# Kernel tuning notes

Measured on AMD Instinct MI355X. Metric: run time of the kernel, lower is better.

## Reference

```python
import jax, jax.numpy as jnp
import numpy as np

B, N, FEAT, H, E, L = 4096, 64, 32, 128, 4, 3  # batch, node_num, node feat, hidden_dim, edge_dim, hidden_num


def setup_inputs() -> dict:
    key = jax.random.key(0)
    ks = jax.random.split(key, 12)
    s = 0.05
    x = jax.random.normal(ks[0], (B, N, FEAT), dtype=jnp.float32)
    adj = jax.random.uniform(ks[1], (B, E, N, N), dtype=jnp.float32)
    # per-node input/output embeddings (stacked over node index)
    in_w = jax.random.normal(ks[2], (N, FEAT, H), dtype=jnp.float32) * s
    in_b = jax.random.normal(ks[3], (N, H), dtype=jnp.float32) * s
    out_w = jax.random.normal(ks[4], (N, H, FEAT), dtype=jnp.float32) * s
    out_b = jax.random.normal(ks[5], (N, FEAT), dtype=jnp.float32) * s
    # relational GC weights per layer: (L, E, H, H) and bias (L, E, 1, H)
    gc_w = jax.random.normal(ks[6], (L, E, H, H), dtype=jnp.float32) * s
    gc_b = jax.random.normal(ks[7], (L, E, 1, H), dtype=jnp.float32) * s
    # GRU params, gate order [r, z, n] like torch
    w_ih = jax.random.normal(ks[8], (3 * H, H), dtype=jnp.float32) * s
    w_hh = jax.random.normal(ks[9], (3 * H, H), dtype=jnp.float32) * s
    b_ih = jax.random.normal(ks[10], (3 * H,), dtype=jnp.float32) * s
    b_hh = jax.random.normal(ks[11], (3 * H,), dtype=jnp.float32) * s
    return {"x": x, "adj": adj, "in_w": in_w, "in_b": in_b, "out_w": out_w,
            "out_b": out_b, "gc_w": gc_w, "gc_b": gc_b, "w_ih": w_ih,
            "w_hh": w_hh, "b_ih": b_ih, "b_hh": b_hh}


def _gru_step(xf, h, w_ih, w_hh, b_ih, b_hh):
    # xf, h: (B*N, H); single-timestep torch GRU cell
    gi = xf @ w_ih.T + b_ih
    gh = h @ w_hh.T + b_hh
    i_r, i_z, i_n = jnp.split(gi, 3, axis=-1)
    h_r, h_z, h_n = jnp.split(gh, 3, axis=-1)
    r = jax.nn.sigmoid(i_r + h_r)
    z = jax.nn.sigmoid(i_z + h_z)
    n = jnp.tanh(i_n + r * h_n)
    return (1.0 - z) * n + z * h


def reference(x, adj, in_w, in_b, out_w, out_b, gc_w, gc_b, w_ih, w_hh, b_ih, b_hh):
    # per-node input embedding: (B, N, FEAT) -> (B, N, H)
    h = jnp.einsum('bnd,ndh->bnh', x, in_w) + in_b
    hidden = h.reshape(-1, H)  # initial GRU hidden = embedded input
    cur = h
    for i in range(L):
        # relational GCN: per-edge-type projection + adjacency matmul + bias + relu + mean over edge types
        support = jnp.einsum('bid,edh->beih', cur, gc_w[i])
        out = jnp.einsum('beij,bejh->beih', adj, support) + gc_b[i]
        out = jax.nn.relu(out)
        agg = jnp.mean(out, axis=1)  # (B, N, H)
        hidden = _gru_step(agg.reshape(-1, H), hidden, w_ih, w_hh, b_ih, b_hh)
        cur = hidden.reshape(B, N, H)
    # per-node output embedding, zero-padded back to hidden width
    feats = jnp.einsum('bnh,nhd->bnd', cur, out_w) + out_b  # (B, N, FEAT)
    return jnp.pad(feats, ((0, 0), (0, 0), (0, H - FEAT)))
```

## Files before the change

### kernel.cpp

```cpp
#include <hip/hip_runtime.h>
#include <cstdint>

#define NBATCH 4096
#define NNODE  64
#define FEAT   32
#define H      128
#define NE     4
#define NL     3

typedef __attribute__((ext_vector_type(8))) short short8;
typedef __attribute__((ext_vector_type(4))) short short4v;
typedef __attribute__((ext_vector_type(4))) float f32x4;
typedef __attribute__((ext_vector_type(2))) float f32x2;
typedef unsigned long long u64;

#define IMG_GC_ELEMS   (128 * 64)
#define IMG_GRU_ELEMS  (48 * 128)
#define IMG_GC_BYTES   (24 * IMG_GC_ELEMS * 2)
#define IMG_GRU_BYTES  (16 * IMG_GRU_ELEMS * 2)
#define WS_W_BYTES     (IMG_GC_BYTES + IMG_GRU_BYTES)
#define WIMG_SHORTS    (WS_W_BYTES / 2)
#define ADJ_IMG_ELEMS  4096
#define WS_FULL ((size_t)WS_W_BYTES + (size_t)NBATCH * NE * ADJ_IMG_ELEMS * 2)

__device__ __forceinline__ unsigned short f2b(float f) {
  union { float f; unsigned u; } v; v.f = f;
  unsigned u = v.u + 0x7FFFu + ((v.u >> 16) & 1u);
  return (unsigned short)(u >> 16);
}
__device__ __forceinline__ float b2f(unsigned short s) {
  union { unsigned u; float f; } v; v.u = ((unsigned)s) << 16;
  return v.f;
}
__device__ __forceinline__ unsigned cvtpk(float lo, float hi) {
  unsigned r;
  asm volatile("v_cvt_pk_bf16_f32 %0, %1, %2" : "=v"(r) : "v"(lo), "v"(hi));
  return r;
}
__device__ __forceinline__ float sigm(float v) { return 1.0f / (1.0f + __expf(-v)); }
__device__ __forceinline__ float tanh_(float v) {
  v = fminf(fmaxf(v, -15.f), 15.f);
  float e = __expf(-2.f * v);
  return (1.f - e) / (1.f + e);
}
__device__ __forceinline__ int gidx128(int r, int g) { return r * 128 + ((g ^ (r & 7)) << 3); }
__device__ __forceinline__ int idx128(int r, int k) { return gidx128(r, k >> 3) + (k & 7); }
__device__ __forceinline__ int gidx64(int r, int g) { return r * 64 + (((g ^ (r & 7)) & 7) << 3); }

__device__ __forceinline__ short8 pack8f(const float* v) {
  union { unsigned u[4]; short8 s; } r;
  r.u[0] = cvtpk(v[0], v[1]); r.u[1] = cvtpk(v[2], v[3]);
  r.u[2] = cvtpk(v[4], v[5]); r.u[3] = cvtpk(v[6], v[7]);
  return r.s;
}

__device__ __forceinline__ void gll16(const void* g, void* l) {
  __builtin_amdgcn_global_load_lds(
      (const __attribute__((address_space(1))) unsigned int*)g,
      (__attribute__((address_space(3))) unsigned int*)l, 16, 0, 0);
}

#define STAGE(dst, src, NIT)                                             \
  do {                                                                   \
    _Pragma("unroll")                                                    \
    for (int it_ = 0; it_ < (NIT); ++it_) {                              \
      int off_ = (it_ * 4 + w) * 1024;                                   \
      gll16((const char*)(src) + off_ + lane * 16, (char*)(dst) + off_); \
    }                                                                    \
  } while (0)

#define BAR() do { asm volatile("s_waitcnt lgkmcnt(0)" ::: "memory"); \
                   __builtin_amdgcn_s_barrier(); } while (0)
#define VMW(N) do { asm volatile("s_waitcnt vmcnt(" #N ")" ::: "memory"); \
                    __builtin_amdgcn_sched_barrier(0); } while (0)
#define SB0() __builtin_amdgcn_sched_barrier(0)

__global__ __launch_bounds__(256, 2) void k_prep(
    const float* __restrict__ gc_w, const float* __restrict__ w_ih,
    const float* __restrict__ w_hh, unsigned short* __restrict__ ws)
{
  const int t = threadIdx.x;
  if (blockIdx.x < 24) {
    const int blk = blockIdx.x;
    const int kh = blk & 1, e = (blk >> 1) & 3, l = blk >> 3;
    const float* We = gc_w + (size_t)(l * NE + e) * H * H;
    unsigned short* dst = ws + (size_t)blk * IMG_GC_ELEMS;
    #pragma unroll
    for (int it = 0; it < 4; ++it) {
      int idx = t + it * 256;
      int r = idx >> 3, g = idx & 7;
      float v[8];
      #pragma unroll
      for (int j = 0; j < 8; ++j) v[j] = We[(kh * 64 + g * 8 + j) * H + r];
      *(short8*)&dst[gidx64(r, g)] = pack8f(v);
    }
  } else {
    const int blk = blockIdx.x - 24;
    const int c = blk & 7, m = blk >> 3;
    const float* Mat = m ? w_hh : w_ih;
    unsigned short* dst = ws + WIMG_SHORTS - IMG_GRU_BYTES / 2 + (size_t)blk * IMG_GRU_ELEMS;
    #pragma unroll
    for (int it = 0; it < 3; ++it) {
      int idx = t + it * 256;
      int rr = idx >> 4, g = idx & 15;
      int mrow = (rr >> 4) * H + 16 * c + (rr & 15);
      float v[8];
      #pragma unroll
      for (int j = 0; j < 8; ++j) v[j] = Mat[mrow * H + g * 8 + j];
      *(short8*)&dst[gidx128(rr, g)] = pack8f(v);
    }
  }
}

template <bool ADJIMG>
__global__ __launch_bounds__(256, 2) void k_inemb(
    const float* __restrict__ x, const float* __restrict__ in_w,
    const float* __restrict__ in_b, const float* __restrict__ adj,
    unsigned short* __restrict__ ws, float* __restrict__ out)
{
  __shared__ float s_wt[FEAT * H];
  __shared__ float s_x[64 * FEAT];
  const int t = threadIdx.x;
  const int n = blockIdx.x >> 6, bt = blockIdx.x & 63, b0 = bt * 64;
  const float* wsrc = in_w + (size_t)n * FEAT * H;
  #pragma unroll
  for (int it = 0; it < 4; ++it) {
    int i4 = t + it * 256;
    *(f32x4*)&s_wt[i4 * 4] = *(const f32x4*)&wsrc[i4 * 4];
  }
  {
    int r = t >> 2, q = t & 3;
    const float* xs = x + ((size_t)(b0 + r) * NNODE + n) * FEAT;
    *(f32x4*)&s_x[r * 32 + q * 8]     = *(const f32x4*)&xs[q * 8];
    *(f32x4*)&s_x[r * 32 + q * 8 + 4] = *(const f32x4*)&xs[q * 8 + 4];
  }
  __syncthreads();
  const int h2 = t & 63, rp = t >> 6;
  const float bi0 = in_b[n * H + 2 * h2], bi1 = in_b[n * H + 2 * h2 + 1];
  #pragma unroll 1
  for (int m = 0; m < 16; ++m) {
    int r = rp + 4 * m;
    float a0 = bi0, a1 = bi1;
    #pragma unroll
    for (int d = 0; d < 32; ++d) {
      float xv = s_x[r * 32 + d];
      f32x2 wv = *(const f32x2*)&s_wt[d * H + 2 * h2];
      a0 += xv * wv.x; a1 += xv * wv.y;
    }
    unsigned p = cvtpk(a0, a1);
    unsigned short* tail = (unsigned short*)(out + ((size_t)(b0 + r) * NNODE + n) * H + 64);
    *(unsigned*)(tail + 2 * h2) = p;
  }
  if (ADJIMG) {
    const float* ab = adj + (size_t)blockIdx.x * NE * NNODE * NNODE;
    unsigned short* dst = ws + WIMG_SHORTS + (size_t)blockIdx.x * NE * ADJ_IMG_ELEMS;
    #pragma unroll 1
    for (int q = 0; q < 8; ++q) {
      int gi = t + q * 256;
      int e = gi >> 9, idx = gi & 511, r = idx >> 3, g = idx & 7;
      const float* src = ab + e * 4096 + r * 64 + g * 8;
      float v[8];
      #pragma unroll
      for (int j = 0; j < 8; ++j) v[j] = src[j];
      *(short8*)&dst[e * ADJ_IMG_ELEMS + gidx64(r, g)] = pack8f(v);
    }
  }
}

template <bool ADJIMG>
__global__ __launch_bounds__(256, 2) void k_main(
    const float* __restrict__ adj,
    const float* __restrict__ gc_b,
    const float* __restrict__ b_ih, const float* __restrict__ b_hh,
    const unsigned short* __restrict__ wimg,
    float* __restrict__ out)
{
  __shared__ unsigned short s_cur[64 * 128];
  __shared__ unsigned short s_u[128 * 64];
  __shared__ unsigned short s_w0[128 * 64];
  __shared__ unsigned short s_w1[128 * 64];
  __shared__ unsigned short s_adj[64 * 64];
  __shared__ float s_bias[1280];

  const int t = threadIdx.x;
  const int b = blockIdx.x;
  const int w = t >> 6, lane = t & 63, lr = lane & 15, lq = lane >> 4;
  float* outb = out + (size_t)b * NNODE * H;
  const unsigned short* img_gru = wimg + WIMG_SHORTS - IMG_GRU_BYTES / 2;
  const unsigned short* aimg = wimg + WIMG_SHORTS + (size_t)b * NE * ADJ_IMG_ELEMS;

  STAGE(s_w0, wimg, 4);
  #pragma unroll
  for (int it = 0; it < 4; ++it) {
    int idx = t + it * 256;
    int n = idx >> 4, g = idx & 15;
    short8 v = *(const short8*)((const unsigned short*)(outb + n * H + 64) + g * 8);
    *(short8*)&s_cur[gidx128(n, g)] = v;
  }
  #pragma unroll
  for (int it = 0; it < 3; ++it) {
    int idx = t + it * 256;
    s_bias[512 + idx] = (idx < 384) ? b_ih[idx] : b_hh[idx - 384];
  }
  __syncthreads();

  #pragma unroll 1
  for (int layer = 0; layer < NL; ++layer) {
    f32x4 agg[8];
    #pragma unroll
    for (int tn = 0; tn < 8; ++tn) agg[tn] = f32x4{0.f, 0.f, 0.f, 0.f};

    #pragma unroll 1
    for (int e = 0; e < NE; ++e) {
      const unsigned short* img_e = wimg + (size_t)((layer * NE + e) * 2) * IMG_GC_ELEMS;

      if (e == 0) {
        s_bias[t]       = gc_b[layer * 512 + t];
        s_bias[t + 256] = gc_b[layer * 512 + t + 256];
      }
      STAGE(s_w1, img_e + IMG_GC_ELEMS, 4);
      SB0();
      if (ADJIMG) {
        STAGE(s_adj, aimg + (size_t)e * ADJ_IMG_ELEMS, 2);
        SB0();
      } else {
        const float* adj_e = adj + (((size_t)b * NE + e) * NNODE * NNODE);
        #pragma unroll
        for (int it = 0; it < 2; ++it) {
          int idx = t + it * 256;
          int i = idx >> 3, g = idx & 7;
          const float* src = adj_e + i * 64 + g * 8;
          float v[8];
          #pragma unroll
          for (int j = 0; j < 8; ++j) v[j] = src[j];
          *(short8*)&s_adj[gidx64(i, g)] = pack8f(v);
        }
      }
      f32x4 Sacc[8];
      #pragma unroll
      for (int tn = 0; tn < 8; ++tn) Sacc[tn] = f32x4{0.f, 0.f, 0.f, 0.f};
      __builtin_amdgcn_s_setprio(1);
      #pragma unroll
      for (int ks = 0; ks < 2; ++ks) {
        short8 a = *(const short8*)&s_cur[gidx128(16 * w + lr, ks * 4 + lq)];
        #pragma unroll
        for (int tn = 0; tn < 8; ++tn) {
          short8 bb = *(const short8*)&s_w0[gidx64(16 * tn + lr, ks * 4 + lq)];
          Sacc[tn] = __builtin_amdgcn_mfma_f32_16x16x32_bf16(a, bb, Sacc[tn], 0, 0, 0);
        }
      }
      __builtin_amdgcn_s_setprio(0);
      if (ADJIMG) { VMW(2); }
      else        { VMW(0); }
      BAR();

      if (e < 3) { STAGE(s_w0, img_e + 2 * IMG_GC_ELEMS, 4); }
      else       { STAGE(s_w0, img_gru, 3); }
      SB0();
      __builtin_amdgcn_s_setprio(1);
      #pragma unroll
      for (int ks = 0; ks < 2; ++ks) {
        short8 a = *(const short8*)&s_cur[gidx128(16 * w + lr, 8 + ks * 4 + lq)];
        #pragma unroll
        for (int tn = 0; tn < 8; ++tn) {
          short8 bb = *(const short8*)&s_w1[gidx64(16 * tn + lr, ks * 4 + lq)];
          Sacc[tn] = __builtin_amdgcn_mfma_f32_16x16x32_bf16(a, bb, Sacc[tn], 0, 0, 0);
        }
      }
      __builtin_amdgcn_s_setprio(0);
      {
        int nb = 16 * w + 4 * lq;
        int g = nb >> 3, sub = nb & 7;
        #pragma unroll
        for (int tn = 0; tn < 8; ++tn) {
          int h = 16 * tn + lr;
          u64 pv = (u64)cvtpk(Sacc[tn][0], Sacc[tn][1]) |
                   ((u64)cvtpk(Sacc[tn][2], Sacc[tn][3]) << 32);
          *(u64*)&s_u[gidx64(h, g) + sub] = pv;
        }
      }
      VMW(4);
      BAR();

      {
        f32x4 Oacc[8];
        #pragma unroll
        for (int tn = 0; tn < 8; ++tn) Oacc[tn] = f32x4{0.f, 0.f, 0.f, 0.f};
        __builtin_amdgcn_s_setprio(1);
        #pragma unroll
        for (int ks = 0; ks < 2; ++ks) {
          short8 a = *(const short8*)&s_adj[gidx64(16 * w + lr, ks * 4 + lq)];
          #pragma unroll
          for (int tn = 0; tn < 8; ++tn) {
            short8 bb = *(const short8*)&s_u[gidx64(16 * tn + lr, ks * 4 + lq)];
            Oacc[tn] = __builtin_amdgcn_mfma_f32_16x16x32_bf16(a, bb, Oacc[tn], 0, 0, 0);
          }
        }
        __builtin_amdgcn_s_setprio(0);
        #pragma unroll
        for (int tn = 0; tn < 8; ++tn) {
          float bias = s_bias[e * 128 + 16 * tn + lr];
          #pragma unroll
          for (int r = 0; r < 4; ++r)
            agg[tn][r] += 0.25f * fmaxf(Oacc[tn][r] + bias, 0.f);
        }
      }
      VMW(0);
      BAR();
    }

    #pragma unroll
    for (int tn = 0; tn < 8; ++tn) {
      int h = 16 * tn + lr;
      #pragma unroll
      for (int r = 0; r < 4; ++r) {
        int i = 16 * w + 4 * lq + r;
        s_u[idx128(i, h)] = f2b(agg[tn][r]);
      }
    }
    BAR();

    #pragma unroll 1
    for (int c = 0; c < 8; ++c) {
      STAGE(s_w1, img_gru + (size_t)(8 + c) * IMG_GRU_ELEMS, 3);
      f32x4 gi[3], gh[3];
      #pragma unroll
      for (int tg = 0; tg < 3; ++tg) gi[tg] = f32x4{0.f, 0.f, 0.f, 0.f};
      __builtin_amdgcn_s_setprio(1);
      #pragma unroll
      for (int ks = 0; ks < 4; ++ks) {
        short8 bb = *(const short8*)&s_u[gidx128(16 * w + lr, ks * 4 + lq)];
        #pragma unroll
        for (int tg = 0; tg < 3; ++tg) {
          short8 a = *(const short8*)&s_w0[gidx128(16 * tg + lr, ks * 4 + lq)];
          gi[tg] = __builtin_amdgcn_mfma_f32_16x16x32_bf16(a, bb, gi[tg], 0, 0, 0);
        }
      }
      __builtin_amdgcn_s_setprio(0);
      __syncthreads();

      if (c < 7)          { STAGE(s_w0, img_gru + (size_t)(c + 1) * IMG_GRU_ELEMS, 3); }
      else if (layer < 2) { STAGE(s_w0, wimg + (size_t)((layer + 1) * NE * 2) * IMG_GC_ELEMS, 4); }
      #pragma unroll
      for (int tg = 0; tg < 3; ++tg) gh[tg] = f32x4{0.f, 0.f, 0.f, 0.f};
      __builtin_amdgcn_s_setprio(1);
      #pragma unroll
      for (int ks = 0; ks < 4; ++ks) {
        short8 bb = *(const short8*)&s_cur[gidx128(16 * w + lr, ks * 4 + lq)];
        #pragma unroll
        for (int tg = 0; tg < 3; ++tg) {
          short8 a = *(const short8*)&s_w1[gidx128(16 * tg + lr, ks * 4 + lq)];
          gh[tg] = __builtin_amdgcn_mfma_f32_16x16x32_bf16(a, bb, gh[tg], 0, 0, 0);
        }
      }
      __builtin_amdgcn_s_setprio(0);
      {
        int i = 16 * w + lr;
        int g = (16 * c + 4 * lq) >> 3;
        int off = gidx128(i, g) + ((4 * lq) & 7);
        short4v hv = *(const short4v*)&s_cur[off];
        float hf[4];
        #pragma unroll
        for (int r = 0; r < 4; ++r) {
          int mH = 16 * c + 4 * lq + r;
          float rg = sigm(gi[0][r] + s_bias[512 + mH] + gh[0][r] + s_bias[896 + mH]);
          float zg = sigm(gi[1][r] + s_bias[640 + mH] + gh[1][r] + s_bias[1024 + mH]);
          float ng = tanh_(gi[2][r] + s_bias[768 + mH] + rg * (gh[2][r] + s_bias[1152 + mH]));
          float hold = b2f((unsigned short)hv[r]);
          hf[r] = (1.f - zg) * ng + zg * hold;
        }
        u64 hp = (u64)cvtpk(hf[0], hf[1]) | ((u64)cvtpk(hf[2], hf[3]) << 32);
        unsigned short* tail = (unsigned short*)(outb + (size_t)i * H + 64);
        *(u64*)(tail + 16 * c + 4 * lq) = hp;
      }
      __syncthreads();
    }

    if (layer < 2) {
      #pragma unroll
      for (int it = 0; it < 4; ++it) {
        int idx = t + it * 256;
        int n = idx >> 4, g = idx & 15;
        short8 v = *(const short8*)((const unsigned short*)(outb + n * H + 64) + g * 8);
        *(short8*)&s_cur[gidx128(n, g)] = v;
      }
      __syncthreads();
    }
  }
}

__global__ __launch_bounds__(256, 2) void k_outemb(
    const float* __restrict__ out_w, const float* __restrict__ out_b,
    float* __restrict__ out)
{
  __shared__ float s_wt[H * FEAT];
  __shared__ float s_c[64 * 132];
  const int t = threadIdx.x;
  const int n = blockIdx.x >> 6, bt = blockIdx.x & 63, b0 = bt * 64;
  const float* wsrc = out_w + (size_t)n * H * FEAT;
  #pragma unroll
  for (int it = 0; it < 4; ++it) {
    int i4 = t + it * 256;
    *(f32x4*)&s_wt[i4 * 4] = *(const f32x4*)&wsrc[i4 * 4];
  }
  #pragma unroll
  for (int it = 0; it < 4; ++it) {
    int idx = t + it * 256;
    int r = idx >> 4, g = idx & 15;
    const unsigned short* tail =
        (const unsigned short*)(out + ((size_t)(b0 + r) * NNODE + n) * H + 64);
    short8 v = *(const short8*)(tail + g * 8);
    #pragma unroll
    for (int j = 0; j < 8; ++j) s_c[r * 132 + g * 8 + j] = b2f((unsigned short)v[j]);
  }
  __syncthreads();
  const int d = t & 31, rq = t >> 5;
  const float bias = out_b[n * FEAT + d];
  float accs[8];
  #pragma unroll
  for (int m = 0; m < 8; ++m) {
    int r = rq + 8 * m;
    float a = bias;
    #pragma unroll 8
    for (int k = 0; k < H; ++k) a += s_c[r * 132 + k] * s_wt[k * FEAT + d];
    accs[m] = a;
  }
  #pragma unroll
  for (int m = 0; m < 8; ++m) {
    int r = rq + 8 * m;
    out[((size_t)(b0 + r) * NNODE + n) * H + d] = accs[m];
  }
  #pragma unroll
  for (int q = 0; q < 6; ++q) {
    int idx = t + q * 256;
    int r = idx / 24, c4 = idx - r * 24;
    *(f32x4*)&out[((size_t)(b0 + r) * NNODE + n) * H + FEAT + c4 * 4] =
        f32x4{0.f, 0.f, 0.f, 0.f};
  }
}

extern "C" void kernel_launch(void* const* d_in, const int* in_sizes, int n_in,
                              void* d_out, int out_size, void* d_ws, size_t ws_size,
                              hipStream_t stream) {
  const float* x     = (const float*)d_in[0];
  const float* adj   = (const float*)d_in[1];
  const float* in_w  = (const float*)d_in[2];
  const float* in_b  = (const float*)d_in[3];
  const float* out_w = (const float*)d_in[4];
  const float* out_b = (const float*)d_in[5];
  const float* gc_w  = (const float*)d_in[6];
  const float* gc_b  = (const float*)d_in[7];
  const float* w_ih  = (const float*)d_in[8];
  const float* w_hh  = (const float*)d_in[9];
  const float* b_ih  = (const float*)d_in[10];
  const float* b_hh  = (const float*)d_in[11];
  (void)in_sizes; (void)n_in; (void)out_size;
  unsigned short* wimg = (unsigned short*)d_ws;
  const bool full = ws_size >= WS_FULL;
  hipLaunchKernelGGL(k_prep, dim3(40), dim3(256), 0, stream, gc_w, w_ih, w_hh, wimg);
  if (full) {
    hipLaunchKernelGGL(k_inemb<true>, dim3(NBATCH), dim3(256), 0, stream,
                       x, in_w, in_b, adj, wimg, (float*)d_out);
    hipLaunchKernelGGL(k_main<true>, dim3(NBATCH), dim3(256), 0, stream,
                       adj, gc_b, b_ih, b_hh, wimg, (float*)d_out);
  } else {
    hipLaunchKernelGGL(k_inemb<false>, dim3(NBATCH), dim3(256), 0, stream,
                       x, in_w, in_b, adj, wimg, (float*)d_out);
    hipLaunchKernelGGL(k_main<false>, dim3(NBATCH), dim3(256), 0, stream,
                       adj, gc_b, b_ih, b_hh, wimg, (float*)d_out);
  }
  hipLaunchKernelGGL(k_outemb, dim3(NBATCH), dim3(256), 0, stream, out_w, out_b, (float*)d_out);
}
```

Before: 823.8 us.

## Retile main kernel MFMAs into 2x2 warp grid with register-held current state

The per-warp work split in the main GCN/GRU kernel changes from 16-row strips over all columns to a 2x2 warp grid (32 rows by 64 columns per warp), so each B fragment loaded from LDS feeds two MFMAs. The current hidden state is kept in registers instead of an LDS tile. The GRU loop now processes two weight chunks per iteration, with separate warp pairs handling each. LDS buffers are merged into one aliased staging area with adjusted vmcnt waits. This aims to cut LDS traffic and barriers, and the smaller LDS footprint may allow more occupancy. In exchange it raises register pressure and makes the async-copy wait counts more fragile.

```diff
diff --git a/kernel.cpp b/kernel.cpp
--- a/kernel.cpp
+++ b/kernel.cpp
@@ -13,6 +13,7 @@
 typedef __attribute__((ext_vector_type(4))) float f32x4;
 typedef __attribute__((ext_vector_type(2))) float f32x2;
 typedef unsigned long long u64;
+typedef unsigned short ushort;
 
 #define IMG_GC_ELEMS   (128 * 64)
 #define IMG_GRU_ELEMS  (48 * 128)
@@ -23,12 +24,12 @@
 #define ADJ_IMG_ELEMS  4096
 #define WS_FULL ((size_t)WS_W_BYTES + (size_t)NBATCH * NE * ADJ_IMG_ELEMS * 2)
 
-__device__ __forceinline__ unsigned short f2b(float f) {
+__device__ __forceinline__ ushort f2b(float f) {
   union { float f; unsigned u; } v; v.f = f;
   unsigned u = v.u + 0x7FFFu + ((v.u >> 16) & 1u);
-  return (unsigned short)(u >> 16);
-}
-__device__ __forceinline__ float b2f(unsigned short s) {
+  return (ushort)(u >> 16);
+}
+__device__ __forceinline__ float b2f(ushort s) {
   union { unsigned u; float f; } v; v.u = ((unsigned)s) << 16;
   return v.f;
 }
@@ -36,6 +37,9 @@
   unsigned r;
   asm volatile("v_cvt_pk_bf16_f32 %0, %1, %2" : "=v"(r) : "v"(lo), "v"(hi));
   return r;
+}
+__device__ __forceinline__ u64 pk4(float a, float b, float c, float d) {
+  return (u64)cvtpk(a, b) | ((u64)cvtpk(c, d) << 32);
 }
 __device__ __forceinline__ float sigm(float v) { return 1.0f / (1.0f + __expf(-v)); }
 __device__ __forceinline__ float tanh_(float v) {
@@ -77,14 +81,14 @@
 
 __global__ __launch_bounds__(256, 2) void k_prep(
     const float* __restrict__ gc_w, const float* __restrict__ w_ih,
-    const float* __restrict__ w_hh, unsigned short* __restrict__ ws)
+    const float* __restrict__ w_hh, ushort* __restrict__ ws)
 {
   const int t = threadIdx.x;
   if (blockIdx.x < 24) {
     const int blk = blockIdx.x;
     const int kh = blk & 1, e = (blk >> 1) & 3, l = blk >> 3;
     const float* We = gc_w + (size_t)(l * NE + e) * H * H;
-    unsigned short* dst = ws + (size_t)blk * IMG_GC_ELEMS;
+    ushort* dst = ws + (size_t)blk * IMG_GC_ELEMS;
     #pragma unroll
     for (int it = 0; it < 4; ++it) {
       int idx = t + it * 256;
@@ -98,7 +102,7 @@
     const int blk = blockIdx.x - 24;
     const int c = blk & 7, m = blk >> 3;
     const float* Mat = m ? w_hh : w_ih;
-    unsigned short* dst = ws + WIMG_SHORTS - IMG_GRU_BYTES / 2 + (size_t)blk * IMG_GRU_ELEMS;
+    ushort* dst = ws + WIMG_SHORTS - IMG_GRU_BYTES / 2 + (size_t)blk * IMG_GRU_ELEMS;
     #pragma unroll
     for (int it = 0; it < 3; ++it) {
       int idx = t + it * 256;
@@ -116,7 +120,7 @@
 __global__ __launch_bounds__(256, 2) void k_inemb(
     const float* __restrict__ x, const float* __restrict__ in_w,
     const float* __restrict__ in_b, const float* __restrict__ adj,
-    unsigned short* __restrict__ ws, float* __restrict__ out)
+    ushort* __restrict__ ws, float* __restrict__ out)
 {
   __shared__ float s_wt[FEAT * H];
   __shared__ float s_x[64 * FEAT];
@@ -148,12 +152,12 @@
       a0 += xv * wv.x; a1 += xv * wv.y;
     }
     unsigned p = cvtpk(a0, a1);
-    unsigned short* tail = (unsigned short*)(out + ((size_t)(b0 + r) * NNODE + n) * H + 64);
+    ushort* tail = (ushort*)(out + ((size_t)(b0 + r) * NNODE + n) * H + 64);
     *(unsigned*)(tail + 2 * h2) = p;
   }
   if (ADJIMG) {
     const float* ab = adj + (size_t)blockIdx.x * NE * NNODE * NNODE;
-    unsigned short* dst = ws + WIMG_SHORTS + (size_t)blockIdx.x * NE * ADJ_IMG_ELEMS;
+    ushort* dst = ws + WIMG_SHORTS + (size_t)blockIdx.x * NE * ADJ_IMG_ELEMS;
     #pragma unroll 1
     for (int q = 0; q < 8; ++q) {
       int gi = t + q * 256;
@@ -172,31 +176,36 @@
     const float* __restrict__ adj,
     const float* __restrict__ gc_b,
     const float* __restrict__ b_ih, const float* __restrict__ b_hh,
-    const unsigned short* __restrict__ wimg,
+    const ushort* __restrict__ wimg,
     float* __restrict__ out)
 {
-  __shared__ unsigned short s_cur[64 * 128];
-  __shared__ unsigned short s_u[128 * 64];
-  __shared__ unsigned short s_w0[128 * 64];
-  __shared__ unsigned short s_w1[128 * 64];
-  __shared__ unsigned short s_adj[64 * 64];
+  __shared__ ushort s_u[128 * 64];
+  __shared__ ushort s_stage[24576];
   __shared__ float s_bias[1280];
+
+  ushort* w0    = s_stage;
+  ushort* w1    = s_stage + 8192;
+  ushort* sadj  = s_stage + 16384;
+  ushort* gru0  = s_stage;
+  ushort* gru1  = s_stage + 12288;
 
   const int t = threadIdx.x;
   const int b = blockIdx.x;
   const int w = t >> 6, lane = t & 63, lr = lane & 15, lq = lane >> 4;
+  const int wm = w & 1, wn = w >> 1;
   float* outb = out + (size_t)b * NNODE * H;
-  const unsigned short* img_gru = wimg + WIMG_SHORTS - IMG_GRU_BYTES / 2;
-  const unsigned short* aimg = wimg + WIMG_SHORTS + (size_t)b * NE * ADJ_IMG_ELEMS;
-
-  STAGE(s_w0, wimg, 4);
-  #pragma unroll
-  for (int it = 0; it < 4; ++it) {
-    int idx = t + it * 256;
-    int n = idx >> 4, g = idx & 15;
-    short8 v = *(const short8*)((const unsigned short*)(outb + n * H + 64) + g * 8);
-    *(short8*)&s_cur[gidx128(n, g)] = v;
-  }
+  const ushort* img_gru = wimg + WIMG_SHORTS - IMG_GRU_BYTES / 2;
+  const ushort* aimg = wimg + WIMG_SHORTS + (size_t)b * NE * ADJ_IMG_ELEMS;
+
+  STAGE(w0, wimg, 4);
+  short8 cur[2][4];
+  #pragma unroll
+  for (int rt = 0; rt < 2; ++rt)
+    #pragma unroll
+    for (int ks = 0; ks < 4; ++ks) {
+      int node = 32 * wm + 16 * rt + lr;
+      cur[rt][ks] = *(const short8*)((const ushort*)(outb + (size_t)node * H + 64) + 32 * ks + 8 * lq);
+    }
   #pragma unroll
   for (int it = 0; it < 3; ++it) {
     int idx = t + it * 256;
@@ -206,22 +215,24 @@
 
   #pragma unroll 1
   for (int layer = 0; layer < NL; ++layer) {
-    f32x4 agg[8];
-    #pragma unroll
-    for (int tn = 0; tn < 8; ++tn) agg[tn] = f32x4{0.f, 0.f, 0.f, 0.f};
+    f32x4 agg[2][4];
+    #pragma unroll
+    for (int mt = 0; mt < 2; ++mt)
+      #pragma unroll
+      for (int nt = 0; nt < 4; ++nt) agg[mt][nt] = f32x4{0.f, 0.f, 0.f, 0.f};
 
     #pragma unroll 1
     for (int e = 0; e < NE; ++e) {
-      const unsigned short* img_e = wimg + (size_t)((layer * NE + e) * 2) * IMG_GC_ELEMS;
+      const ushort* img_e = wimg + (size_t)((layer * NE + e) * 2) * IMG_GC_ELEMS;
 
       if (e == 0) {
         s_bias[t]       = gc_b[layer * 512 + t];
         s_bias[t + 256] = gc_b[layer * 512 + t + 256];
       }
-      STAGE(s_w1, img_e + IMG_GC_ELEMS, 4);
+      STAGE(w1, img_e + IMG_GC_ELEMS, 4);
       SB0();
       if (ADJIMG) {
-        STAGE(s_adj, aimg + (size_t)e * ADJ_IMG_ELEMS, 2);
+        STAGE(sadj, aimg + (size_t)e * ADJ_IMG_ELEMS, 2);
         SB0();
       } else {
         const float* adj_e = adj + (((size_t)b * NE + e) * NNODE * NNODE);
@@ -233,158 +244,191 @@
           float v[8];
           #pragma unroll
           for (int j = 0; j < 8; ++j) v[j] = src[j];
-          *(short8*)&s_adj[gidx64(i, g)] = pack8f(v);
-        }
-      }
-      f32x4 Sacc[8];
-      #pragma unroll
-      for (int tn = 0; tn < 8; ++tn) Sacc[tn] = f32x4{0.f, 0.f, 0.f, 0.f};
+          *(short8*)&sadj[gidx64(i, g)] = pack8f(v);
+        }
+      }
+      f32x4 Sacc[2][4];
+      #pragma unroll
+      for (int mt = 0; mt < 2; ++mt)
+        #pragma unroll
+        for (int nt = 0; nt < 4; ++nt) Sacc[mt][nt] = f32x4{0.f, 0.f, 0.f, 0.f};
+      if (ADJIMG) VMW(6);
       __builtin_amdgcn_s_setprio(1);
       #pragma unroll
       for (int ks = 0; ks < 2; ++ks) {
-        short8 a = *(const short8*)&s_cur[gidx128(16 * w + lr, ks * 4 + lq)];
-        #pragma unroll
-        for (int tn = 0; tn < 8; ++tn) {
-          short8 bb = *(const short8*)&s_w0[gidx64(16 * tn + lr, ks * 4 + lq)];
-          Sacc[tn] = __builtin_amdgcn_mfma_f32_16x16x32_bf16(a, bb, Sacc[tn], 0, 0, 0);
+        #pragma unroll
+        for (int nt = 0; nt < 4; ++nt) {
+          short8 bb = *(const short8*)&w0[gidx64(64 * wn + 16 * nt + lr, ks * 4 + lq)];
+          #pragma unroll
+          for (int mt = 0; mt < 2; ++mt)
+            Sacc[mt][nt] = __builtin_amdgcn_mfma_f32_16x16x32_bf16(cur[mt][ks], bb, Sacc[mt][nt], 0, 0, 0);
         }
       }
       __builtin_amdgcn_s_setprio(0);
-      if (ADJIMG) { VMW(2); }
-      else        { VMW(0); }
-      BAR();
-
-      if (e < 3) { STAGE(s_w0, img_e + 2 * IMG_GC_ELEMS, 4); }
-      else       { STAGE(s_w0, img_gru, 3); }
+      if (ADJIMG) { VMW(2); BAR(); } else __syncthreads();
+
+      if (e < 3) { STAGE(w0, img_e + 2 * IMG_GC_ELEMS, 4); }
+      else       { STAGE(gru0, img_gru, 3); }
       SB0();
       __builtin_amdgcn_s_setprio(1);
       #pragma unroll
       for (int ks = 0; ks < 2; ++ks) {
-        short8 a = *(const short8*)&s_cur[gidx128(16 * w + lr, 8 + ks * 4 + lq)];
-        #pragma unroll
-        for (int tn = 0; tn < 8; ++tn) {
-          short8 bb = *(const short8*)&s_w1[gidx64(16 * tn + lr, ks * 4 + lq)];
-          Sacc[tn] = __builtin_amdgcn_mfma_f32_16x16x32_bf16(a, bb, Sacc[tn], 0, 0, 0);
+        #pragma unroll
+        for (int nt = 0; nt < 4; ++nt) {
+          short8 bb = *(const short8*)&w1[gidx64(64 * wn + 16 * nt + lr, ks * 4 + lq)];
+          #pragma unroll
+          for (int mt = 0; mt < 2; ++mt)
+            Sacc[mt][nt] = __builtin_amdgcn_mfma_f32_16x16x32_bf16(cur[mt][2 + ks], bb, Sacc[mt][nt], 0, 0, 0);
         }
       }
       __builtin_amdgcn_s_setprio(0);
+      #pragma unroll
+      for (int mt = 0; mt < 2; ++mt) {
+        int j0 = 32 * wm + 16 * mt + 4 * lq;
+        #pragma unroll
+        for (int nt = 0; nt < 4; ++nt) {
+          int h = 64 * wn + 16 * nt + lr;
+          *(u64*)&s_u[gidx64(h, j0 >> 3) + (j0 & 7)] =
+              pk4(Sacc[mt][nt][0], Sacc[mt][nt][1], Sacc[mt][nt][2], Sacc[mt][nt][3]);
+        }
+      }
+      if (ADJIMG) { if (e < 3) { VMW(4); } else { VMW(3); } BAR(); } else __syncthreads();
+
+      if (e == 3) { STAGE(gru0 + 6144, img_gru + IMG_GRU_ELEMS, 3); SB0(); }
       {
-        int nb = 16 * w + 4 * lq;
-        int g = nb >> 3, sub = nb & 7;
-        #pragma unroll
-        for (int tn = 0; tn < 8; ++tn) {
-          int h = 16 * tn + lr;
-          u64 pv = (u64)cvtpk(Sacc[tn][0], Sacc[tn][1]) |
-                   ((u64)cvtpk(Sacc[tn][2], Sacc[tn][3]) << 32);
-          *(u64*)&s_u[gidx64(h, g) + sub] = pv;
-        }
-      }
-      VMW(4);
-      BAR();
-
-      {
-        f32x4 Oacc[8];
-        #pragma unroll
-        for (int tn = 0; tn < 8; ++tn) Oacc[tn] = f32x4{0.f, 0.f, 0.f, 0.f};
+        f32x4 Oacc[2][4];
+        #pragma unroll
+        for (int mt = 0; mt < 2; ++mt)
+          #pragma unroll
+          for (int nt = 0; nt < 4; ++nt) Oacc[mt][nt] = f32x4{0.f, 0.f, 0.f, 0.f};
         __builtin_amdgcn_s_setprio(1);
         #pragma unroll
         for (int ks = 0; ks < 2; ++ks) {
-          short8 a = *(const short8*)&s_adj[gidx64(16 * w + lr, ks * 4 + lq)];
-          #pragma unroll
-          for (int tn = 0; tn < 8; ++tn) {
-            short8 bb = *(const short8*)&s_u[gidx64(16 * tn + lr, ks * 4 + lq)];
-            Oacc[tn] = __builtin_amdgcn_mfma_f32_16x16x32_bf16(a, bb, Oacc[tn], 0, 0, 0);
+          short8 a[2];
+          #pragma unroll
+          for (int mt = 0; mt < 2; ++mt)
+            a[mt] = *(const short8*)&sadj[gidx64(32 * wm + 16 * mt + lr, ks * 4 + lq)];
+          #pragma unroll
+          for (int nt = 0; nt < 4; ++nt) {
+            short8 bb = *(const short8*)&s_u[gidx64(64 * wn + 16 * nt + lr, ks * 4 + lq)];
+            #pragma unroll
+            for (int mt = 0; mt < 2; ++mt)
+              Oacc[mt][nt] = __builtin_amdgcn_mfma_f32_16x16x32_bf16(a[mt], bb, Oacc[mt][nt], 0, 0, 0);
           }
         }
         __builtin_amdgcn_s_setprio(0);
         #pragma unroll
-        for (int tn = 0; tn < 8; ++tn) {
-          float bias = s_bias[e * 128 + 16 * tn + lr];
-          #pragma unroll
-          for (int r = 0; r < 4; ++r)
-            agg[tn][r] += 0.25f * fmaxf(Oacc[tn][r] + bias, 0.f);
-        }
-      }
-      VMW(0);
-      BAR();
-    }
-
-    #pragma unroll
-    for (int tn = 0; tn < 8; ++tn) {
-      int h = 16 * tn + lr;
-      #pragma unroll
-      for (int r = 0; r < 4; ++r) {
-        int i = 16 * w + 4 * lq + r;
-        s_u[idx128(i, h)] = f2b(agg[tn][r]);
-      }
-    }
-    BAR();
+        for (int mt = 0; mt < 2; ++mt)
+          #pragma unroll
+          for (int nt = 0; nt < 4; ++nt) {
+            float bias = s_bias[e * 128 + 64 * wn + 16 * nt + lr];
+            #pragma unroll
+            for (int r = 0; r < 4; ++r)
+              agg[mt][nt][r] += 0.25f * fmaxf(Oacc[mt][nt][r] + bias, 0.f);
+          }
+      }
+      if (ADJIMG) { BAR(); } else __syncthreads();
+    }
+
+    #pragma unroll
+    for (int mt = 0; mt < 2; ++mt)
+      #pragma unroll
+      for (int nt = 0; nt < 4; ++nt) {
+        int h = 64 * wn + 16 * nt + lr;
+        #pragma unroll
+        for (int r = 0; r < 4; ++r)
+          s_u[idx128(32 * wm + 16 * mt + 4 * lq + r, h)] = f2b(agg[mt][nt][r]);
+      }
+    __syncthreads();
 
     #pragma unroll 1
-    for (int c = 0; c < 8; ++c) {
-      STAGE(s_w1, img_gru + (size_t)(8 + c) * IMG_GRU_ELEMS, 3);
-      f32x4 gi[3], gh[3];
-      #pragma unroll
-      for (int tg = 0; tg < 3; ++tg) gi[tg] = f32x4{0.f, 0.f, 0.f, 0.f};
+    for (int p = 0; p < 4; ++p) {
+      const int cc = 2 * p + wn;
+      const ushort* ihb = gru0 + wn * 6144;
+      const ushort* hhb = gru1 + wn * 6144;
+      STAGE(gru1, img_gru + (size_t)(8 + 2 * p) * IMG_GRU_ELEMS, 3);
+      STAGE(gru1 + 6144, img_gru + (size_t)(8 + 2 * p + 1) * IMG_GRU_ELEMS, 3);
+      SB0();
+      short4v holdv[2];
+      #pragma unroll
+      for (int nst = 0; nst < 2; ++nst) {
+        int node = 16 * (2 * wm + nst) + lr;
+        holdv[nst] = *(const short4v*)((const ushort*)(outb + (size_t)node * H + 64) + 16 * cc + 4 * lq);
+      }
+      f32x4 gi[3][2];
+      #pragma unroll
+      for (int tg = 0; tg < 3; ++tg)
+        #pragma unroll
+        for (int nst = 0; nst < 2; ++nst) gi[tg][nst] = f32x4{0.f, 0.f, 0.f, 0.f};
       __builtin_amdgcn_s_setprio(1);
       #pragma unroll
       for (int ks = 0; ks < 4; ++ks) {
-        short8 bb = *(const short8*)&s_u[gidx128(16 * w + lr, ks * 4 + lq)];
+        short8 bb[2];
+        #pragma unroll
+        for (int nst = 0; nst < 2; ++nst)
+          bb[nst] = *(const short8*)&s_u[gidx128(16 * (2 * wm + nst) + lr, ks * 4 + lq)];
         #pragma unroll
         for (int tg = 0; tg < 3; ++tg) {
-          short8 a = *(const short8*)&s_w0[gidx128(16 * tg + lr, ks * 4 + lq)];
-          gi[tg] = __builtin_amdgcn_mfma_f32_16x16x32_bf16(a, bb, gi[tg], 0, 0, 0);
+          short8 a = *(const short8*)&ihb[gidx128(16 * tg + lr, ks * 4 + lq)];
+          #pragma unroll
+          for (int nst = 0; nst < 2; ++nst)
+            gi[tg][nst] = __builtin_amdgcn_mfma_f32_16x16x32_bf16(a, bb[nst], gi[tg][nst], 0, 0, 0);
         }
       }
       __builtin_amdgcn_s_setprio(0);
       __syncthreads();
 
-      if (c < 7)          { STAGE(s_w0, img_gru + (size_t)(c + 1) * IMG_GRU_ELEMS, 3); }
-      else if (layer < 2) { STAGE(s_w0, wimg + (size_t)((layer + 1) * NE * 2) * IMG_GC_ELEMS, 4); }
-      #pragma unroll
-      for (int tg = 0; tg < 3; ++tg) gh[tg] = f32x4{0.f, 0.f, 0.f, 0.f};
+      if (p < 3) {
+        STAGE(gru0, img_gru + (size_t)(2 * (p + 1)) * IMG_GRU_ELEMS, 3);
+        STAGE(gru0 + 6144, img_gru + (size_t)(2 * (p + 1) + 1) * IMG_GRU_ELEMS, 3);
+      } else if (layer < 2) {
+        STAGE(w0, wimg + (size_t)((layer + 1) * NE * 2) * IMG_GC_ELEMS, 4);
+      }
+      SB0();
+      f32x4 gh[3][2];
+      #pragma unroll
+      for (int tg = 0; tg < 3; ++tg)
+        #pragma unroll
+        for (int nst = 0; nst < 2; ++nst) gh[tg][nst] = f32x4{0.f, 0.f, 0.f, 0.f};
       __builtin_amdgcn_s_setprio(1);
       #pragma unroll
       for (int ks = 0; ks < 4; ++ks) {
-        short8 bb = *(const short8*)&s_cur[gidx128(16 * w + lr, ks * 4 + lq)];
         #pragma unroll
         for (int tg = 0; tg < 3; ++tg) {
-          short8 a = *(const short8*)&s_w1[gidx128(16 * tg + lr, ks * 4 + lq)];
-          gh[tg] = __builtin_amdgcn_mfma_f32_16x16x32_bf16(a, bb, gh[tg], 0, 0, 0);
+          short8 a = *(const short8*)&hhb[gidx128(16 * tg + lr, ks * 4 + lq)];
+          #pragma unroll
+          for (int nst = 0; nst < 2; ++nst)
+            gh[tg][nst] = __builtin_amdgcn_mfma_f32_16x16x32_bf16(a, cur[nst][ks], gh[tg][nst], 0, 0, 0);
         }
       }
       __builtin_amdgcn_s_setprio(0);
-      {
-        int i = 16 * w + lr;
-        int g = (16 * c + 4 * lq) >> 3;
-        int off = gidx128(i, g) + ((4 * lq) & 7);
-        short4v hv = *(const short4v*)&s_cur[off];
+      #pragma unroll
+      for (int nst = 0; nst < 2; ++nst) {
+        int node = 16 * (2 * wm + nst) + lr;
         float hf[4];
         #pragma unroll
         for (int r = 0; r < 4; ++r) {
-          int mH = 16 * c + 4 * lq + r;
-          float rg = sigm(gi[0][r] + s_bias[512 + mH] + gh[0][r] + s_bias[896 + mH]);
-          float zg = sigm(gi[1][r] + s_bias[640 + mH] + gh[1][r] + s_bias[1024 + mH]);
-          float ng = tanh_(gi[2][r] + s_bias[768 + mH] + rg * (gh[2][r] + s_bias[1152 + mH]));
-          float hold = b2f((unsigned short)hv[r]);
+          int mH = 16 * cc + 4 * lq + r;
+          float rg = sigm(gi[0][nst][r] + s_bias[512 + mH] + gh[0][nst][r] + s_bias[896 + mH]);
+          float zg = sigm(gi[1][nst][r] + s_bias[640 + mH] + gh[1][nst][r] + s_bias[1024 + mH]);
+          float ng = tanh_(gi[2][nst][r] + s_bias[768 + mH] + rg * (gh[2][nst][r] + s_bias[1152 + mH]));
+          float hold = b2f((ushort)holdv[nst][r]);
           hf[r] = (1.f - zg) * ng + zg * hold;
         }
-        u64 hp = (u64)cvtpk(hf[0], hf[1]) | ((u64)cvtpk(hf[2], hf[3]) << 32);
-        unsigned short* tail = (unsigned short*)(outb + (size_t)i * H + 64);
-        *(u64*)(tail + 16 * c + 4 * lq) = hp;
+        *(u64*)((ushort*)(outb + (size_t)node * H + 64) + 16 * cc + 4 * lq) =
+            pk4(hf[0], hf[1], hf[2], hf[3]);
       }
       __syncthreads();
     }
 
     if (layer < 2) {
       #pragma unroll
-      for (int it = 0; it < 4; ++it) {
-        int idx = t + it * 256;
-        int n = idx >> 4, g = idx & 15;
-        short8 v = *(const short8*)((const unsigned short*)(outb + n * H + 64) + g * 8);
-        *(short8*)&s_cur[gidx128(n, g)] = v;
-      }
-      __syncthreads();
+      for (int rt = 0; rt < 2; ++rt)
+        #pragma unroll
+        for (int ks = 0; ks < 4; ++ks) {
+          int node = 32 * wm + 16 * rt + lr;
+          cur[rt][ks] = *(const short8*)((const ushort*)(outb + (size_t)node * H + 64) + 32 * ks + 8 * lq);
+        }
     }
   }
 }
@@ -407,11 +451,10 @@
   for (int it = 0; it < 4; ++it) {
     int idx = t + it * 256;
     int r = idx >> 4, g = idx & 15;
-    const unsigned short* tail =
-        (const unsigned short*)(out + ((size_t)(b0 + r) * NNODE + n) * H + 64);
+    const ushort* tail = (const ushort*)(out + ((size_t)(b0 + r) * NNODE + n) * H + 64);
     short8 v = *(const short8*)(tail + g * 8);
     #pragma unroll
-    for (int j = 0; j < 8; ++j) s_c[r * 132 + g * 8 + j] = b2f((unsigned short)v[j]);
+    for (int j = 0; j < 8; ++j) s_c[r * 132 + g * 8 + j] = b2f((ushort)v[j]);
   }
   __syncthreads();
   const int d = t & 31, rq = t >> 5;
@@ -455,7 +498,7 @@
   const float* b_ih  = (const float*)d_in[10];
   const float* b_hh  = (const float*)d_in[11];
   (void)in_sizes; (void)n_in; (void)out_size;
-  unsigned short* wimg = (unsigned short*)d_ws;
+  ushort* wimg = (ushort*)d_ws;
   const bool full = ws_size >= WS_FULL;
   hipLaunchKernelGGL(k_prep, dim3(40), dim3(256), 0, stream, gc_w, w_ih, w_hh, wimg);
   if (full) {
```

Result: faster. 763.9 us, median of 2 (-7.3%).
